# Optimization experiments

Measured on AMD Instinct MI355X. Metric: run time of the kernel, lower is better.

The kernel has to match this reference:

```python
import jax, jax.numpy as jnp
import numpy as np

B, L, D = 4, 2048, 512
H, DK = 8, 64          # n_heads, d_k = d_model // n_heads
DF = 2048              # d_ff
W = 9                  # window_size (odd so padding w//2 keeps L windows)


def setup_inputs() -> dict:
    key = jax.random.key(0)
    ks = jax.random.split(key, 12)
    s = 0.02
    p = lambda k, shp: (jax.random.normal(k, shp, jnp.float32) * s)
    return {
        "x": jax.random.normal(ks[0], (B, L, D), jnp.float32),
        "Wq": p(ks[1], (D, D)), "bq": jnp.zeros((D,), jnp.float32),
        "Wk": p(ks[2], (D, D)), "bk": jnp.zeros((D,), jnp.float32),
        "Wv": p(ks[3], (D, D)), "bv": jnp.zeros((D,), jnp.float32),
        "Wo": p(ks[4], (D, D)), "bo": jnp.zeros((D,), jnp.float32),
        "W1": p(ks[5], (D, DF)), "b1": jnp.zeros((DF,), jnp.float32),
        "W2": p(ks[6], (DF, D)), "b2": jnp.zeros((D,), jnp.float32),
        "g1": jnp.ones((D,), jnp.float32), "be1": jnp.zeros((D,), jnp.float32),
        "g2": jnp.ones((D,), jnp.float32), "be2": jnp.zeros((D,), jnp.float32),
    }


def _layer_norm(x, g, b, eps=1e-5):
    m = jnp.mean(x, axis=-1, keepdims=True)
    v = jnp.var(x, axis=-1, keepdims=True)
    return (x - m) * jax.lax.rsqrt(v + eps) * g + b


def reference(x, Wq, bq, Wk, bk, Wv, bv, Wo, bo, W1, b1, W2, b2, g1, be1, g2, be2):
    b, l, d = x.shape
    pad = W // 2
    padded = jnp.pad(x, ((0, 0), (pad, pad), (0, 0)))          # (B, L+W-1, D)
    idx = jnp.arange(l)[:, None] + jnp.arange(W)[None, :]       # (L, W)
    win = padded[:, idx]                                        # (B, L, W, D)

    # per-window full attention (Informer FullAttention, mask_flag=False)
    q = (win @ Wq + bq).reshape(b, l, W, H, DK)
    k = (win @ Wk + bk).reshape(b, l, W, H, DK)
    v = (win @ Wv + bv).reshape(b, l, W, H, DK)
    scale = 1.0 / jnp.sqrt(jnp.float32(DK))
    scores = jnp.einsum('blqhe,blkhe->blhqk', q, k) * scale     # (B, L, H, W, W)
    attn = jax.nn.softmax(scores, axis=-1)
    o = jnp.einsum('blhqk,blkhd->blqhd', attn, v).reshape(b, l, W, d)
    o = o @ Wo + bo                                             # (B, L, W, D)
    new_x = jnp.mean(o, axis=2)                                 # mean-pool over window

    x1 = _layer_norm(x + new_x, g1, be1)

    # pointwise conv FFN (kernel_size=1 Conv1d == Linear), exact GELU
    h = jax.nn.gelu(x1 @ W1 + b1, approximate=False)
    y = h @ W2 + b2
    return _layer_norm(x1 + y, g2, be2)
```

## Files before the change

### kernel.cpp

```cpp
#include <hip/hip_runtime.h>


typedef unsigned short u16;
typedef __attribute__((ext_vector_type(8))) short short8;
typedef __attribute__((ext_vector_type(4))) float floatx4;

#define DEV static __device__ __forceinline__

DEV float b2f(u16 u) {
  union { unsigned int i; float f; } x; x.i = ((unsigned int)u) << 16; return x.f;
}
DEV u16 f2b(float f) {
  union { float f; unsigned int i; } x; x.f = f;
  unsigned int u = x.i + 0x7fffu + ((x.i >> 16) & 1u);
  return (u16)(u >> 16);
}

#define AS1 __attribute__((address_space(1)))
#define AS3 __attribute__((address_space(3)))
DEV void gload_lds16(const void* g, void* l) {
  __builtin_amdgcn_global_load_lds((const AS1 void*)g, (AS3 void*)l, 16, 0, 0);
}

__global__ __launch_bounds__(256) void prep_weights(
    const float* __restrict__ Wq, const float* __restrict__ Wk,
    const float* __restrict__ Wo, const float* __restrict__ W1,
    const float* __restrict__ W2, const float* __restrict__ Wv,
    u16* __restrict__ WqkvT, u16* __restrict__ WoT,
    u16* __restrict__ W1T, u16* __restrict__ W2T, u16* __restrict__ Wvb) {
  const int bid = blockIdx.x;
  if (bid >= 2816) {
    const int i = (bid - 2816) * 256 + threadIdx.x;
    float4 v = ((const float4*)Wv)[i];
    ushort4 o;
    o.x = f2b(v.x); o.y = f2b(v.y); o.z = f2b(v.z); o.w = f2b(v.w);
    ((ushort4*)Wvb)[i] = o;
    return;
  }
  const float* in; u16* out; int R, C, t;
  if (bid < 256)       { in = Wq; out = WqkvT;          R = 512;  C = 512;  t = bid; }
  else if (bid < 512)  { in = Wk; out = WqkvT + 262144; R = 512;  C = 512;  t = bid - 256; }
  else if (bid < 768)  { in = Wo; out = WoT;            R = 512;  C = 512;  t = bid - 512; }
  else if (bid < 1792) { in = W1; out = W1T;            R = 512;  C = 2048; t = bid - 768; }
  else                 { in = W2; out = W2T;            R = 2048; C = 512;  t = bid - 1792; }
  const int tpr = C >> 5;
  const int bc = (t % tpr) * 32, br = (t / tpr) * 32;
  __shared__ float tile[32][33];
  const int tx = threadIdx.x & 31, ty = threadIdx.x >> 5;
  #pragma unroll
  for (int i = 0; i < 32; i += 8)
    tile[ty + i][tx] = in[(size_t)(br + ty + i) * C + bc + tx];
  __syncthreads();
  #pragma unroll
  for (int i = 0; i < 32; i += 8)
    out[(size_t)(bc + ty + i) * R + br + tx] = f2b(tile[tx][ty + i]);
}

__global__ __launch_bounds__(256) void bias_prep(
    const float* __restrict__ bq, const float* __restrict__ bk,
    const float* __restrict__ bv, const float* __restrict__ Wo,
    float* __restrict__ o) {
  const int i = blockIdx.x * 256 + threadIdx.x;
  if (i < 512) o[i] = bq[i];
  else if (i < 1024) o[i] = bk[i - 512];
  else if (i < 1536) {
    const int c = i - 1024;
    float s = 0.f;
    for (int j = 0; j < 512; ++j) s += bv[j] * Wo[(size_t)j * 512 + c];
    o[i] = s;
  } else if (i < 2048) o[i] = 0.f;
}

__global__ __launch_bounds__(256) void f2b_vec(
    const float* __restrict__ in, u16* __restrict__ out, int n4) {
  int i = blockIdx.x * 256 + threadIdx.x;
  if (i < n4) {
    float4 v = ((const float4*)in)[i];
    ushort4 o;
    o.x = f2b(v.x); o.y = f2b(v.y); o.z = f2b(v.z); o.w = f2b(v.w);
    ((ushort4*)out)[i] = o;
  }
}

template<int EPI>
__global__ __launch_bounds__(256, 2) void gemm_bt(
    const u16* __restrict__ A, const u16* __restrict__ BT,
    const float* __restrict__ bias, u16* __restrict__ C,
    int M, int N, int K) {
  __shared__ __align__(16) u16 As[2][128 * 32];
  __shared__ __align__(16) u16 Bs[2][128 * 32];
  const int tid  = threadIdx.x;
  const int wave = tid >> 6, lane = tid & 63;
  const int l15 = lane & 15, l4 = lane >> 4;
  const int bm = blockIdx.y * 128, bn = blockIdx.x * 128;
  const int wm = (wave >> 1) * 64, wn = (wave & 1) * 64;

  floatx4 acc[4][4] = {};

  const int row0 = tid >> 2, kc0 = (tid & 3) * 8;
  const u16* gA = A  + (size_t)(bm + row0) * K + kc0;
  const u16* gB = BT + (size_t)(bn + row0) * K + kc0;
  const int lofs = wave * 512;

  auto stage = [&](int t, int buf) {
    const u16* a = gA + t * 32;
    const u16* b = gB + t * 32;
    gload_lds16(a,                  &As[buf][lofs]);
    gload_lds16(b,                  &Bs[buf][lofs]);
    gload_lds16(a + (size_t)64 * K, &As[buf][lofs + 2048]);
    gload_lds16(b + (size_t)64 * K, &Bs[buf][lofs + 2048]);
  };

  const int nt = K >> 5;
  stage(0, 0);
  asm volatile("s_waitcnt vmcnt(0)" ::: "memory");
  __builtin_amdgcn_s_barrier();

  for (int t = 0; t < nt; ++t) {
    const int cur = t & 1;
    if (t + 1 < nt) stage(t + 1, cur ^ 1);

    short8 af[4], bf4[4];
    #pragma unroll
    for (int i = 0; i < 4; ++i) {
      af[i]  = *(const short8*)(&As[cur][(wm + i * 16 + l15) * 32 + l4 * 8]);
      bf4[i] = *(const short8*)(&Bs[cur][(wn + i * 16 + l15) * 32 + l4 * 8]);
    }
    #pragma unroll
    for (int i = 0; i < 4; ++i)
      #pragma unroll
      for (int j = 0; j < 4; ++j)
        acc[i][j] = __builtin_amdgcn_mfma_f32_16x16x32_bf16(af[i], bf4[j], acc[i][j], 0, 0, 0);

    asm volatile("s_waitcnt vmcnt(0)" ::: "memory");
    __builtin_amdgcn_s_barrier();
  }

  float bv[4];
  #pragma unroll
  for (int j = 0; j < 4; ++j) bv[j] = bias[bn + wn + j * 16 + l15];
  #pragma unroll
  for (int i = 0; i < 4; ++i) {
    #pragma unroll
    for (int r = 0; r < 4; ++r) {
      size_t row = (size_t)(bm + wm + i * 16 + l4 * 4 + r);
      u16* cp = C + row * N + (bn + wn + l15);
      #pragma unroll
      for (int j = 0; j < 4; ++j) {
        float v = acc[i][j][r] + bv[j];
        if (EPI == 1) v = 0.5f * v * (1.0f + erff(v * 0.70710678118654752f));
        cp[j * 16] = f2b(v);
      }
    }
  }
}

#define ATL 32
#define ART (ATL + 8)

__global__ __launch_bounds__(256) void attn_band(
    const u16* __restrict__ QKV, const float* __restrict__ bqkv,
    const float* __restrict__ bo, u16* __restrict__ newx) {
  __shared__ __align__(16) u16 S3[3][ART][72];
  __shared__ float Gb[ART][18];
  __shared__ float Sm[ART][81];
  __shared__ float Wb[ATL][9];

  const int tid = threadIdx.x;
  const int bid = ((int)blockIdx.x & 7) * 256 + ((int)blockIdx.x >> 3);
  const int h = bid & 7;
  const int chunk = (bid >> 3) & 63;
  const int b = bid >> 9;
  const int l0 = chunk * ATL;

  for (int idx = tid; idx < ART * 24; idx += 256) {
    const int ti = idx / 24, c = idx % 24;
    const int slice = c >> 3, d8 = (c & 7) * 8;
    const int col = slice * 512 + h * 64 + d8;
    const int t = l0 - 4 + ti;
    short8 v;
    if ((unsigned)t < 2048u) {
      v = *(const short8*)(QKV + ((size_t)((b << 11) | t)) * 1536 + col);
    } else {
      #pragma unroll
      for (int j = 0; j < 8; ++j) v[j] = (short)f2b(bqkv[col + j]);
    }
    *(short8*)(&S3[slice][ti][d8]) = v;
  }
  __syncthreads();

  for (int task = tid; task < ART * 17; task += 256) {
    const int ti = task / 17, j = task % 17;
    const int ui = ti + j - 8;
    if ((unsigned)ui < (unsigned)ART) {
      float a = 0.f;
      #pragma unroll
      for (int d0 = 0; d0 < 64; d0 += 8) {
        short8 qv = *(const short8*)(&S3[0][ti][d0]);
        short8 kv = *(const short8*)(&S3[1][ui][d0]);
        #pragma unroll
        for (int jj = 0; jj < 8; ++jj) a += b2f((u16)qv[jj]) * b2f((u16)kv[jj]);
      }
      Gb[ti][j] = a * 0.125f;
    }
  }
  __syncthreads();

  for (int task = tid; task < ART * 9; task += 256) {
    const int ti = task / 9, qw = task % 9;
    const int li = ti - qw;
    if ((unsigned)li < (unsigned)ATL) {
      float m = -1e30f;
      #pragma unroll
      for (int kw = 0; kw < 9; ++kw) m = fmaxf(m, Gb[ti][kw - qw + 8]);
      float e[9], s = 0.f;
      #pragma unroll
      for (int kw = 0; kw < 9; ++kw) { e[kw] = expf(Gb[ti][kw - qw + 8] - m); s += e[kw]; }
      const float inv = 1.f / s;
      #pragma unroll
      for (int kw = 0; kw < 9; ++kw) Sm[ti][qw * 9 + kw] = e[kw] * inv;
    }
  }
  __syncthreads();

  for (int task = tid; task < ATL * 9; task += 256) {
    const int li = task / 9, kw = task % 9;
    float s = 0.f;
    #pragma unroll
    for (int qw = 0; qw < 9; ++qw) s += Sm[li + qw][qw * 9 + kw];
    Wb[li][kw] = s * (1.f / 9.f);
  }
  __syncthreads();

  {
    const int li = tid >> 3, d8 = (tid & 7) * 8;
    float w[9];
    #pragma unroll
    for (int kw = 0; kw < 9; ++kw) w[kw] = Wb[li][kw];
    float a[8] = {};
    #pragma unroll
    for (int kw = 0; kw < 9; ++kw) {
      short8 vv = *(const short8*)(&S3[2][li + kw][d8]);
      #pragma unroll
      for (int jj = 0; jj < 8; ++jj) a[jj] += w[kw] * b2f((u16)vv[jj]);
    }
    short8 o;
    #pragma unroll
    for (int jj = 0; jj < 8; ++jj) o[jj] = (short)f2b(a[jj] + bo[h * 64 + d8 + jj]);
    const int l = l0 + li;
    *(short8*)(newx + ((size_t)((b << 11) | l)) * 512 + h * 64 + d8) = o;
  }
}

template<int MODE>
__global__ __launch_bounds__(256) void ln_kernel(
    const float* __restrict__ af, const u16* __restrict__ ab,
    const u16* __restrict__ bb,
    const float* __restrict__ g, const float* __restrict__ be,
    u16* __restrict__ outb, float* __restrict__ outf) {
  const int wave = threadIdx.x >> 6, lane = threadIdx.x & 63;
  const size_t row = (size_t)blockIdx.x * 4 + wave;
  const size_t base = row * 512 + lane * 8;
  const int gi = lane * 8;
  float v[8];
  short8 b8 = *(const short8*)(bb + base);
  if (MODE == 0) {
    float4 a0 = *(const float4*)(af + base);
    float4 a1 = *(const float4*)(af + base + 4);
    v[0] = a0.x; v[1] = a0.y; v[2] = a0.z; v[3] = a0.w;
    v[4] = a1.x; v[5] = a1.y; v[6] = a1.z; v[7] = a1.w;
  } else {
    short8 a8 = *(const short8*)(ab + base);
    #pragma unroll
    for (int j = 0; j < 8; ++j) v[j] = b2f((u16)a8[j]);
  }
  #pragma unroll
  for (int j = 0; j < 8; ++j) v[j] += b2f((u16)b8[j]);

  float s = 0.f;
  #pragma unroll
  for (int j = 0; j < 8; ++j) s += v[j];
  #pragma unroll
  for (int off = 32; off >= 1; off >>= 1) s += __shfl_xor(s, off, 64);
  const float mean = s * (1.f / 512.f);
  float sq = 0.f;
  #pragma unroll
  for (int j = 0; j < 8; ++j) { float d = v[j] - mean; sq += d * d; }
  #pragma unroll
  for (int off = 32; off >= 1; off >>= 1) sq += __shfl_xor(sq, off, 64);
  const float rs = rsqrtf(sq * (1.f / 512.f) + 1e-5f);

  if (MODE == 0) {
    short8 o;
    #pragma unroll
    for (int j = 0; j < 8; ++j)
      o[j] = (short)f2b((v[j] - mean) * rs * g[gi + j] + be[gi + j]);
    *(short8*)(outb + base) = o;
  } else {
    float4 o0, o1;
    o0.x = (v[0] - mean) * rs * g[gi + 0] + be[gi + 0];
    o0.y = (v[1] - mean) * rs * g[gi + 1] + be[gi + 1];
    o0.z = (v[2] - mean) * rs * g[gi + 2] + be[gi + 2];
    o0.w = (v[3] - mean) * rs * g[gi + 3] + be[gi + 3];
    o1.x = (v[4] - mean) * rs * g[gi + 4] + be[gi + 4];
    o1.y = (v[5] - mean) * rs * g[gi + 5] + be[gi + 5];
    o1.z = (v[6] - mean) * rs * g[gi + 6] + be[gi + 6];
    o1.w = (v[7] - mean) * rs * g[gi + 7] + be[gi + 7];
    *(float4*)(outf + base) = o0;
    *(float4*)(outf + base + 4) = o1;
  }
}

extern "C" void kernel_launch(void* const* d_in, const int* in_sizes, int n_in,
                              void* d_out, int out_size, void* d_ws, size_t ws_size,
                              hipStream_t stream) {
  const float* x   = (const float*)d_in[0];
  const float* Wq  = (const float*)d_in[1];
  const float* bq  = (const float*)d_in[2];
  const float* Wk  = (const float*)d_in[3];
  const float* bk  = (const float*)d_in[4];
  const float* Wv  = (const float*)d_in[5];
  const float* bv  = (const float*)d_in[6];
  const float* Wo  = (const float*)d_in[7];
  const float* bo  = (const float*)d_in[8];
  const float* W1  = (const float*)d_in[9];
  const float* b1  = (const float*)d_in[10];
  const float* W2  = (const float*)d_in[11];
  const float* b2  = (const float*)d_in[12];
  const float* g1  = (const float*)d_in[13];
  const float* be1 = (const float*)d_in[14];
  const float* g2  = (const float*)d_in[15];
  const float* be2 = (const float*)d_in[16];

  char* w = (char*)d_ws;
  u16*   xb    = (u16*)  (w + 0);
  u16*   WqkvT = (u16*)  (w + 8388608);
  u16*   WoT   = (u16*)  (w + 9961472);
  u16*   W1T   = (u16*)  (w + 10485760);
  u16*   W2T   = (u16*)  (w + 12582912);
  float* bqkv  = (float*)(w + 14680064);
  u16*   Wvb   = (u16*)  (w + 14688256);
  u16*   QKV   = (u16*)  (w + 15212544);
  u16*   hbuf  = QKV;
  u16*   newx  = (u16*)  (w + 48766976);
  u16*   ybuf  = newx;
  u16*   x1b   = (u16*)  (w + 57155584);
  u16*   WvoT  = WqkvT + 524288;

  prep_weights<<<3072, 256, 0, stream>>>(Wq, Wk, Wo, W1, W2, Wv,
                                         WqkvT, WoT, W1T, W2T, Wvb);
  bias_prep<<<8, 256, 0, stream>>>(bq, bk, bv, Wo, bqkv);
  f2b_vec<<<4096, 256, 0, stream>>>(x, xb, 1048576);
  gemm_bt<0><<<dim3(4, 4), 256, 0, stream>>>(WoT, Wvb, bqkv + 1536, WvoT, 512, 512, 512);
  gemm_bt<0><<<dim3(12, 64), 256, 0, stream>>>(xb, WqkvT, bqkv, QKV, 8192, 1536, 512);
  attn_band<<<2048, 256, 0, stream>>>(QKV, bqkv, bo, newx);
  ln_kernel<0><<<2048, 256, 0, stream>>>(x, nullptr, newx, g1, be1, x1b, nullptr);
  gemm_bt<1><<<dim3(16, 64), 256, 0, stream>>>(x1b, W1T, b1, hbuf, 8192, 2048, 512);
  gemm_bt<0><<<dim3(4, 64), 256, 0, stream>>>(hbuf, W2T, b2, ybuf, 8192, 512, 2048);
  ln_kernel<1><<<2048, 256, 0, stream>>>(nullptr, x1b, ybuf, g2, be2, nullptr, (float*)d_out);
}
```

Measured before the change: 167.2 us.

## Triple-buffer GEMM LDS pipeline with swizzle, XCD block remap, and bf16 LN input

The bf16 GEMM moves from double to triple LDS buffering, keeping two tiles of global-to-LDS loads in flight with partial vmcnt waits. It also XOR-rotates the 16-byte chunk placement in LDS to cut bank conflicts, and remaps workgroup IDs so neighbouring tiles land on the same XCD for L2 reuse. The MFMA section is raised with s_setprio. The first LayerNorm now reads the bf16 copy of x instead of fp32 x, which halves that read but adds a little rounding error. The cost is more LDS per block, which could lower occupancy.

```diff
diff --git a/kernel.cpp b/kernel.cpp
--- a/kernel.cpp
+++ b/kernel.cpp
@@ -87,20 +87,36 @@
     const u16* __restrict__ A, const u16* __restrict__ BT,
     const float* __restrict__ bias, u16* __restrict__ C,
     int M, int N, int K) {
-  __shared__ __align__(16) u16 As[2][128 * 32];
-  __shared__ __align__(16) u16 Bs[2][128 * 32];
+  __shared__ __align__(16) u16 As[3][4096];
+  __shared__ __align__(16) u16 Bs[3][4096];
   const int tid  = threadIdx.x;
   const int wave = tid >> 6, lane = tid & 63;
   const int l15 = lane & 15, l4 = lane >> 4;
-  const int bm = blockIdx.y * 128, bn = blockIdx.x * 128;
+
+  const int nwg = (int)(gridDim.x * gridDim.y);
+  const int id  = (int)(blockIdx.y * gridDim.x + blockIdx.x);
+  const int cpx = nwg >> 3;
+  const int v   = (id & 7) * cpx + (id >> 3);
+  const int bn  = (v % (int)gridDim.x) * 128;
+  const int bm  = (v / (int)gridDim.x) * 128;
   const int wm = (wave >> 1) * 64, wn = (wave & 1) * 64;
 
   floatx4 acc[4][4] = {};
 
-  const int row0 = tid >> 2, kc0 = (tid & 3) * 8;
+  const int row0 = tid >> 2;
+  const int kc0  = ((((tid & 3) - ((tid >> 3) & 3)) & 3)) * 8;
   const u16* gA = A  + (size_t)(bm + row0) * K + kc0;
   const u16* gB = BT + (size_t)(bn + row0) * K + kc0;
   const int lofs = wave * 512;
+
+  int aoff[4], boff[4];
+  #pragma unroll
+  for (int i = 0; i < 4; ++i) {
+    const int ra = wm + i * 16 + l15;
+    aoff[i] = ra * 32 + (((l4 + (ra >> 1)) & 3) << 3);
+    const int rb = wn + i * 16 + l15;
+    boff[i] = rb * 32 + (((l4 + (rb >> 1)) & 3) << 3);
+  }
 
   auto stage = [&](int t, int buf) {
     const u16* a = gA + t * 32;
@@ -113,32 +129,43 @@
 
   const int nt = K >> 5;
   stage(0, 0);
-  asm volatile("s_waitcnt vmcnt(0)" ::: "memory");
+  stage(1, 1);
+  asm volatile("s_waitcnt vmcnt(4)" ::: "memory");
   __builtin_amdgcn_s_barrier();
-
+  asm volatile("" ::: "memory");
+
+  int cur = 0;
   for (int t = 0; t < nt; ++t) {
-    const int cur = t & 1;
-    if (t + 1 < nt) stage(t + 1, cur ^ 1);
-
+    int sb = cur + 2; if (sb >= 3) sb -= 3;
+    if (t + 2 < nt) stage(t + 2, sb);
+
+    const u16* Ab = &As[cur][0];
+    const u16* Bb = &Bs[cur][0];
     short8 af[4], bf4[4];
     #pragma unroll
     for (int i = 0; i < 4; ++i) {
-      af[i]  = *(const short8*)(&As[cur][(wm + i * 16 + l15) * 32 + l4 * 8]);
-      bf4[i] = *(const short8*)(&Bs[cur][(wn + i * 16 + l15) * 32 + l4 * 8]);
-    }
+      af[i]  = *(const short8*)(Ab + aoff[i]);
+      bf4[i] = *(const short8*)(Bb + boff[i]);
+    }
+    __builtin_amdgcn_s_setprio(1);
     #pragma unroll
     for (int i = 0; i < 4; ++i)
       #pragma unroll
       for (int j = 0; j < 4; ++j)
         acc[i][j] = __builtin_amdgcn_mfma_f32_16x16x32_bf16(af[i], bf4[j], acc[i][j], 0, 0, 0);
-
-    asm volatile("s_waitcnt vmcnt(0)" ::: "memory");
+    __builtin_amdgcn_s_setprio(0);
+
+    if (t + 2 < nt) asm volatile("s_waitcnt vmcnt(4)" ::: "memory");
+    else            asm volatile("s_waitcnt vmcnt(0)" ::: "memory");
     __builtin_amdgcn_s_barrier();
-  }
-
-  float bv[4];
-  #pragma unroll
-  for (int j = 0; j < 4; ++j) bv[j] = bias[bn + wn + j * 16 + l15];
+    asm volatile("" ::: "memory");
+
+    cur = (cur == 2) ? 0 : cur + 1;
+  }
+
+  float bvv[4];
+  #pragma unroll
+  for (int j = 0; j < 4; ++j) bvv[j] = bias[bn + wn + j * 16 + l15];
   #pragma unroll
   for (int i = 0; i < 4; ++i) {
     #pragma unroll
@@ -147,9 +174,9 @@
       u16* cp = C + row * N + (bn + wn + l15);
       #pragma unroll
       for (int j = 0; j < 4; ++j) {
-        float v = acc[i][j][r] + bv[j];
-        if (EPI == 1) v = 0.5f * v * (1.0f + erff(v * 0.70710678118654752f));
-        cp[j * 16] = f2b(v);
+        float vv = acc[i][j][r] + bvv[j];
+        if (EPI == 1) vv = 0.5f * vv * (1.0f + erff(vv * 0.70710678118654752f));
+        cp[j * 16] = f2b(vv);
       }
     }
   }
@@ -252,10 +279,9 @@
   }
 }
 
-template<int MODE>
+template<int OUTF>
 __global__ __launch_bounds__(256) void ln_kernel(
-    const float* __restrict__ af, const u16* __restrict__ ab,
-    const u16* __restrict__ bb,
+    const u16* __restrict__ a, const u16* __restrict__ bsrc,
     const float* __restrict__ g, const float* __restrict__ be,
     u16* __restrict__ outb, float* __restrict__ outf) {
   const int wave = threadIdx.x >> 6, lane = threadIdx.x & 63;
@@ -263,19 +289,10 @@
   const size_t base = row * 512 + lane * 8;
   const int gi = lane * 8;
   float v[8];
-  short8 b8 = *(const short8*)(bb + base);
-  if (MODE == 0) {
-    float4 a0 = *(const float4*)(af + base);
-    float4 a1 = *(const float4*)(af + base + 4);
-    v[0] = a0.x; v[1] = a0.y; v[2] = a0.z; v[3] = a0.w;
-    v[4] = a1.x; v[5] = a1.y; v[6] = a1.z; v[7] = a1.w;
-  } else {
-    short8 a8 = *(const short8*)(ab + base);
-    #pragma unroll
-    for (int j = 0; j < 8; ++j) v[j] = b2f((u16)a8[j]);
-  }
-  #pragma unroll
-  for (int j = 0; j < 8; ++j) v[j] += b2f((u16)b8[j]);
+  short8 a8 = *(const short8*)(a + base);
+  short8 b8 = *(const short8*)(bsrc + base);
+  #pragma unroll
+  for (int j = 0; j < 8; ++j) v[j] = b2f((u16)a8[j]) + b2f((u16)b8[j]);
 
   float s = 0.f;
   #pragma unroll
@@ -290,7 +307,7 @@
   for (int off = 32; off >= 1; off >>= 1) sq += __shfl_xor(sq, off, 64);
   const float rs = rsqrtf(sq * (1.f / 512.f) + 1e-5f);
 
-  if (MODE == 0) {
+  if (OUTF == 0) {
     short8 o;
     #pragma unroll
     for (int j = 0; j < 8; ++j)
@@ -354,8 +371,8 @@
   gemm_bt<0><<<dim3(4, 4), 256, 0, stream>>>(WoT, Wvb, bqkv + 1536, WvoT, 512, 512, 512);
   gemm_bt<0><<<dim3(12, 64), 256, 0, stream>>>(xb, WqkvT, bqkv, QKV, 8192, 1536, 512);
   attn_band<<<2048, 256, 0, stream>>>(QKV, bqkv, bo, newx);
-  ln_kernel<0><<<2048, 256, 0, stream>>>(x, nullptr, newx, g1, be1, x1b, nullptr);
+  ln_kernel<0><<<2048, 256, 0, stream>>>(xb, newx, g1, be1, x1b, nullptr);
   gemm_bt<1><<<dim3(16, 64), 256, 0, stream>>>(x1b, W1T, b1, hbuf, 8192, 2048, 512);
   gemm_bt<0><<<dim3(4, 64), 256, 0, stream>>>(hbuf, W2T, b2, ybuf, 8192, 512, 2048);
-  ln_kernel<1><<<2048, 256, 0, stream>>>(nullptr, x1b, ybuf, g2, be2, nullptr, (float*)d_out);
-}
+  ln_kernel<1><<<2048, 256, 0, stream>>>(x1b, ybuf, g2, be2, nullptr, (float*)d_out);
+}
```

Measured after the change: 173.6 us. +3.8%, slower.
